# Kernel tuning notes

Hardware: AMD Instinct MI355X
Metric: run time of the kernel (lower is better)

Reference implementation:

```python
import jax, jax.numpy as jnp
import numpy as np

E, NH, NL, NP = 256, 8, 4, 4
D = E // NH
SPATIAL_SHAPES = np.array([[100, 134], [50, 67], [25, 34], [13, 17]], dtype=np.int64)
B = 2


def setup_inputs() -> dict:
    key = jax.random.key(0)
    ks = jax.random.split(key, 12)
    Lin = int((SPATIAL_SHAPES[:, 0] * SPATIAL_SHAPES[:, 1]).sum())
    Lq = Lin
    s = 0.02
    return {
        'query': jax.random.normal(ks[0], (Lq, B, E), jnp.float32),
        'value': jax.random.normal(ks[1], (Lin, B, E), jnp.float32),
        'reference_points': jax.random.uniform(ks[2], (B, Lq, NL, 2), jnp.float32),
        'spatial_shapes': SPATIAL_SHAPES,
        'W_value': jax.random.normal(ks[3], (E, E), jnp.float32) * s,
        'b_value': jnp.zeros((E,), jnp.float32),
        'W_offset': jax.random.normal(ks[4], (E, NH * NL * NP * 2), jnp.float32) * s,
        'b_offset': jax.random.normal(ks[5], (NH * NL * NP * 2,), jnp.float32) * 0.5,
        'W_attn': jax.random.normal(ks[6], (E, NH * NL * NP), jnp.float32) * s,
        'b_attn': jnp.zeros((NH * NL * NP,), jnp.float32),
        'W_out': jax.random.normal(ks[7], (E, E), jnp.float32) * s,
        'b_out': jnp.zeros((E,), jnp.float32),
    }


def _ms_deform_attn(value, spatial_shapes, sampling_locations, attention_weights):
    # value: (B, Lin, NH, D); sampling_locations: (B, Lq, NH, NL, NP, 2) in [0,1]
    # attention_weights: (B, Lq, NH, NL, NP)
    b, _, nh, d = value.shape
    lq = sampling_locations.shape[1]
    npnt = sampling_locations.shape[4]
    shapes = np.asarray(spatial_shapes)
    out = jnp.zeros((b, nh, lq, d), value.dtype)
    start = 0
    for l in range(shapes.shape[0]):
        H, W = int(shapes[l, 0]), int(shapes[l, 1])
        vl = value[:, start:start + H * W].transpose(0, 2, 1, 3)  # (B, NH, H*W, D)
        loc = sampling_locations[:, :, :, l].transpose(0, 2, 1, 3, 4)  # (B, NH, Lq, P, 2)
        # grid_sample align_corners=False convention (matches CUDA kernel)
        x = loc[..., 0] * W - 0.5
        y = loc[..., 1] * H - 0.5
        x0 = jnp.floor(x)
        y0 = jnp.floor(y)
        dx = x - x0
        dy = y - y0
        x0i = x0.astype(jnp.int32)
        y0i = y0.astype(jnp.int32)
        acc = jnp.zeros((b, nh, lq, npnt, d), value.dtype)
        corners = [
            (x0i, y0i, (1.0 - dx) * (1.0 - dy)),
            (x0i + 1, y0i, dx * (1.0 - dy)),
            (x0i, y0i + 1, (1.0 - dx) * dy),
            (x0i + 1, y0i + 1, dx * dy),
        ]
        for xi, yi, w in corners:
            valid = ((xi >= 0) & (xi < W) & (yi >= 0) & (yi < H)).astype(value.dtype)
            idx = jnp.clip(yi, 0, W - 1 if False else H - 1) * 0  # placeholder removed below
            idx = jnp.clip(yi, 0, H - 1) * W + jnp.clip(xi, 0, W - 1)  # (B, NH, Lq, P)
            g = jnp.take_along_axis(vl, idx.reshape(b, nh, -1)[..., None], axis=2)
            g = g.reshape(b, nh, lq, npnt, d)
            acc = acc + g * (w * valid)[..., None]
        awl = attention_weights[:, :, :, l].transpose(0, 2, 1, 3)  # (B, NH, Lq, P)
        out = out + jnp.einsum('bhqpd,bhqp->bhqd', acc, awl)
        start += H * W
    return out.transpose(0, 2, 1, 3).reshape(b, lq, nh * d)  # (B, Lq, E)


def reference(query, value, reference_points, spatial_shapes,
              W_value, b_value, W_offset, b_offset, W_attn, b_attn, W_out, b_out):
    q = query.transpose(1, 0, 2)   # (B, Lq, E)
    v = value.transpose(1, 0, 2)   # (B, Lin, E)
    b, lq, _ = q.shape
    lin = v.shape[1]
    v = (v @ W_value + b_value).reshape(b, lin, NH, D)
    offsets = (q @ W_offset + b_offset).reshape(b, lq, NH, NL, NP, 2)
    attn = (q @ W_attn + b_attn).reshape(b, lq, NH, NL, NP)
    attn = jax.nn.softmax(attn, axis=-1)  # softmax over points (as in source)
    shapes_f = jnp.asarray(np.asarray(spatial_shapes), jnp.float32)
    offset_normalizer = jnp.stack([shapes_f[:, 1], shapes_f[:, 0]], -1)  # (NL, 2) = (w, h)
    loc = reference_points[:, :, None, :, None, :] + offsets / offset_normalizer[None, None, None, :, None, :]
    out = _ms_deform_attn(v, spatial_shapes, loc, attn)  # (B, Lq, E)
    out = out @ W_out + b_out
    return out.transpose(1, 0, 2)  # (Lq, B, E)
```

## Files before the change

### kernel.cpp

```cpp
#include <hip/hip_runtime.h>
#include <math.h>

#define LQ    17821
#define MROWS 35642
#define KD    256

typedef __attribute__((ext_vector_type(8))) short bf16x8;
typedef __attribute__((ext_vector_type(4))) float f32x4;
typedef unsigned int u32;

__device__ __forceinline__ short f2bf(float f) {
  union { float f; unsigned u; } c; c.f = f;
  unsigned u = c.u;
  return (short)((u + 0x7fffu + ((u >> 16) & 1u)) >> 16);
}
__device__ __forceinline__ float bf2f(short s) {
  union { unsigned u; float f; } c;
  c.u = ((unsigned)(unsigned short)s) << 16;
  return c.f;
}

__device__ __forceinline__ void gld_lds16(const short* g, short* l) {
  __builtin_amdgcn_global_load_lds(
      (const __attribute__((address_space(1))) u32*)g,
      (__attribute__((address_space(3))) u32*)l, 16, 0, 0);
}

#define WAIT_VM4   { __builtin_amdgcn_s_waitcnt(0x0F74); asm volatile("" ::: "memory"); }
#define WAIT_VM0   { __builtin_amdgcn_s_waitcnt(0x0F70); asm volatile("" ::: "memory"); }
#define WAIT_LGKM0 { __builtin_amdgcn_s_waitcnt(0xC07F); asm volatile("" ::: "memory"); }
#define BARRIER    { asm volatile("" ::: "memory"); __builtin_amdgcn_s_barrier(); asm volatile("" ::: "memory"); }

__global__ __launch_bounds__(256) void prep(
    const float* __restrict__ query, const float* __restrict__ value,
    const float* __restrict__ Wv, const float* __restrict__ Woff,
    const float* __restrict__ Wat, const float* __restrict__ Wout,
    const float* __restrict__ boff, const float* __restrict__ bat,
    short* __restrict__ qb, short* __restrict__ vb,
    short* __restrict__ wT, float* __restrict__ fbias)
{
  const int y = blockIdx.y;
  if (y < 2) {
    const float* s = y ? value : query;
    short* d = y ? vb : qb;
    int i = (blockIdx.x * 256 + threadIdx.x) * 4;
    if (i < MROWS * KD) {
      float4 x = *(const float4*)(s + i);
      short4 o;
      o.x = f2bf(x.x); o.y = f2bf(x.y); o.z = f2bf(x.z); o.w = f2bf(x.w);
      *(short4*)(d + i) = o;
    }
    return;
  }
  int idx = blockIdx.x * 256 + threadIdx.x;
  if (idx < 229376) {
    const float* W; int base, N;
    if (idx < 65536)       { W = Wv;   base = 0;      N = 256; }
    else if (idx < 131072) { W = Woff; base = 65536;  N = 256; }
    else if (idx < 163840) { W = Wat;  base = 131072; N = 128; }
    else                   { W = Wout; base = 163840; N = 256; }
    int local = idx - base;
    int n = local >> 8, k = local & 255;
    wT[idx] = f2bf(W[k * N + n]);
  } else if (idx < 229376 + 384) {
    int j = idx - 229376;
    fbias[j] = (j < 256) ? boff[j] : bat[j - 256];
  }
}

template<bool O1BF>
__global__ __launch_bounds__(256) void gemm_pipe(
    const short* __restrict__ A0, const short* __restrict__ A1,
    const short* __restrict__ Bt0, const short* __restrict__ Bt1,
    const float* __restrict__ bias0, const float* __restrict__ bias1,
    short* __restrict__ out0, void* __restrict__ out1v,
    int N1, int gybase)
{
  __shared__ short As[2 * 128 * 32];
  __shared__ short Bs[2 * 128 * 32];

  const int tid = threadIdx.x;
  const int gy = blockIdx.y + gybase;
  const bool sel0 = gy < 2;
  const short* A = sel0 ? A0 : A1;
  const short* Bt = sel0 ? Bt0 : Bt1;
  const float* bias = sel0 ? bias0 : bias1;
  const int bn = (sel0 ? gy : gy - 2) * 128;
  const int bm = blockIdx.x * 128;

  const int wv = tid >> 6;
  const int lane = tid & 63;

  const int srow = lane >> 2;
  const int skel = (lane & 3) * 8;
  const int rA0 = min(bm + wv * 32 + srow, MROWS - 1);
  const int rA1 = min(bm + wv * 32 + 16 + srow, MROWS - 1);
  const short* gA0 = A + (size_t)rA0 * KD + skel;
  const short* gA1 = A + (size_t)rA1 * KD + skel;
  const short* gB0 = Bt + (size_t)(bn + wv * 32 + srow) * KD + skel;
  const short* gB1 = Bt + (size_t)(bn + wv * 32 + 16 + srow) * KD + skel;
  short* lA0 = &As[(wv * 32) * 32];
  short* lA1 = &As[(wv * 32 + 16) * 32];
  short* lB0 = &Bs[(wv * 32) * 32];
  short* lB1 = &Bs[(wv * 32 + 16) * 32];

#define ISSUE(t, buf)                          \
  {                                            \
    gld_lds16(gA0 + (t) * 32, lA0 + (buf) * 4096); \
    gld_lds16(gA1 + (t) * 32, lA1 + (buf) * 4096); \
    gld_lds16(gB0 + (t) * 32, lB0 + (buf) * 4096); \
    gld_lds16(gB1 + (t) * 32, lB1 + (buf) * 4096); \
  }

  const int wm = (wv & 1) * 64;
  const int wn = (wv >> 1) * 64;
  const int ln = lane & 15;
  const int lq = lane >> 4;

  f32x4 acc[4][4];
#pragma unroll
  for (int i = 0; i < 4; ++i)
#pragma unroll
    for (int j = 0; j < 4; ++j) acc[i][j] = (f32x4){0.f, 0.f, 0.f, 0.f};

  ISSUE(0, 0);
  ISSUE(1, 1);

#pragma unroll
  for (int t = 0; t < 8; ++t) {
    const int buf = t & 1;
    if (t < 7) { WAIT_VM4; } else { WAIT_VM0; }
    BARRIER;

    bf16x8 af[4], bfm[4];
#pragma unroll
    for (int i = 0; i < 4; ++i)
      af[i] = *(const bf16x8*)&As[buf * 4096 + (wm + i * 16 + ln) * 32 + lq * 8];
#pragma unroll
    for (int j = 0; j < 4; ++j)
      bfm[j] = *(const bf16x8*)&Bs[buf * 4096 + (wn + j * 16 + ln) * 32 + lq * 8];

    WAIT_LGKM0;
    BARRIER;
    if (t + 2 < 8) ISSUE(t + 2, buf);

#pragma unroll
    for (int i = 0; i < 4; ++i)
#pragma unroll
      for (int j = 0; j < 4; ++j)
        acc[i][j] = __builtin_amdgcn_mfma_f32_16x16x32_bf16(af[i], bfm[j], acc[i][j], 0, 0, 0);
  }
#undef ISSUE

  const int N = sel0 ? 256 : N1;
#pragma unroll
  for (int j = 0; j < 4; ++j) {
    const int col = bn + wn + j * 16 + ln;
    const float bb = bias[col];
#pragma unroll
    for (int i = 0; i < 4; ++i) {
      const int row0 = bm + wm + i * 16 + lq * 4;
#pragma unroll
      for (int r = 0; r < 4; ++r) {
        const int row = row0 + r;
        if (row < MROWS) {
          float v = acc[i][j][r] + bb;
          if (sel0)
            out0[(size_t)row * 256 + col] = f2bf(v);
          else if (O1BF)
            ((short*)out1v)[(size_t)row * N + col] = f2bf(v);
          else
            ((float*)out1v)[(size_t)row * N + col] = v;
        }
      }
    }
  }
}

__global__ __launch_bounds__(256) void msda_sample(
    const short* __restrict__ vproj, const short* __restrict__ oa,
    const float* __restrict__ refp, short* __restrict__ out)
{
  static constexpr int LVL_H[4] = {100, 50, 25, 13};
  static constexpr int LVL_W[4] = {134, 67, 34, 17};
  static constexpr int LVL_S[4] = {0, 13400, 16750, 17600};

  __shared__ uint4 s_pk[8 * 8 * 17];

  const int tid = threadIdx.x;
  const int m0 = blockIdx.x * 8;

#pragma unroll
  for (int it = 0; it < 4; ++it) {
    int w = tid + it * 256;
    int mr = w >> 7;
    int rest = w & 127;
    int h = rest >> 4;
    int lp = rest & 15;
    int l = lp >> 2;
    int p = lp & 3;
    int m = m0 + mr;
    if (m < MROWS) {
      int b = m & 1, q = m >> 1;
      const int Hl = LVL_H[l], Wl = LVL_W[l], Sl = LVL_S[l];
      const float fW = (float)Wl, fH = (float)Hl;

      short4 a4 = *(const short4*)(oa + (size_t)m * 384 + 256 + h * 16 + l * 4);
      float a0 = bf2f(a4.x), a1 = bf2f(a4.y), a2 = bf2f(a4.z), a3 = bf2f(a4.w);
      float mx = fmaxf(fmaxf(a0, a1), fmaxf(a2, a3));
      a0 = __expf(a0 - mx); a1 = __expf(a1 - mx);
      a2 = __expf(a2 - mx); a3 = __expf(a3 - mx);
      float sel = (p == 0) ? a0 : (p == 1) ? a1 : (p == 2) ? a2 : a3;
      float aw = sel / (a0 + a1 + a2 + a3);

      const short* oPtr = oa + (size_t)m * 384 + h * 32 + l * 8 + p * 2;
      float ox = bf2f(oPtr[0]), oy = bf2f(oPtr[1]);
      const float* rPtr = refp + ((size_t)b * LQ + q) * 8 + l * 2;
      float rx = rPtr[0], ry = rPtr[1];

      float x = (rx + ox / fW) * fW - 0.5f;
      float y = (ry + oy / fH) * fH - 0.5f;
      float x0f = floorf(x), y0f = floorf(y);
      float dx = x - x0f, dy = y - y0f;
      int x0 = (int)x0f, y0 = (int)y0f;
      int x1 = x0 + 1, y1 = y0 + 1;

      float w00 = (1.f - dx) * (1.f - dy) * aw;
      float w10 = dx * (1.f - dy) * aw;
      float w01 = (1.f - dx) * dy * aw;
      float w11 = dx * dy * aw;

      bool vx0 = (x0 >= 0) & (x0 < Wl);
      bool vx1 = (x1 >= 0) & (x1 < Wl);
      bool vy0 = (y0 >= 0) & (y0 < Hl);
      bool vy1 = (y1 >= 0) & (y1 < Hl);
      int cx0 = min(max(x0, 0), Wl - 1);
      int cx1 = min(max(x1, 0), Wl - 1);
      int cy0 = min(max(y0, 0), Hl - 1);
      int cy1 = min(max(y1, 0), Hl - 1);

      int r0 = Sl + cy0 * Wl;
      int r1 = Sl + cy1 * Wl;

      float f00 = (vy0 & vx0) ? w00 : 0.f;
      float f10 = (vy0 & vx1) ? w10 : 0.f;
      float f01 = (vy1 & vx0) ? w01 : 0.f;
      float f11 = (vy1 & vx1) ? w11 : 0.f;
      u32 pk0 = (u32)((r0 + cx0) * 2 + b) |
                ((u32)__builtin_bit_cast(unsigned short, (_Float16)f00) << 16);
      u32 pk1 = (u32)((r0 + cx1) * 2 + b) |
                ((u32)__builtin_bit_cast(unsigned short, (_Float16)f10) << 16);
      u32 pk2 = (u32)((r1 + cx0) * 2 + b) |
                ((u32)__builtin_bit_cast(unsigned short, (_Float16)f01) << 16);
      u32 pk3 = (u32)((r1 + cx1) * 2 + b) |
                ((u32)__builtin_bit_cast(unsigned short, (_Float16)f11) << 16);
      int e = (mr * 8 + h) * 17 + lp;
      s_pk[e] = make_uint4(pk0, pk1, pk2, pk3);
    }
  }
  __syncthreads();

  const int mr = tid >> 5;
  const int t = tid & 31;
  const int h = t >> 2;
  const int dq = t & 3;
  const int m = m0 + mr;
  if (m >= MROWS) return;

  const int laneOff = h * 32 + dq * 8;
  const int ebase = (mr * 8 + h) * 17;
  const short* vp = vproj + laneOff;

  float acc[8];
#pragma unroll
  for (int e = 0; e < 8; ++e) acc[e] = 0.f;

#pragma unroll 4
  for (int lp = 0; lp < 16; ++lp) {
    uint4 pk = s_pk[ebase + lp];
    bf16x8 u00 = *(const bf16x8*)(vp + ((int)(pk.x & 0xFFFFu) << 8));
    bf16x8 u10 = *(const bf16x8*)(vp + ((int)(pk.y & 0xFFFFu) << 8));
    bf16x8 u01 = *(const bf16x8*)(vp + ((int)(pk.z & 0xFFFFu) << 8));
    bf16x8 u11 = *(const bf16x8*)(vp + ((int)(pk.w & 0xFFFFu) << 8));
    float w0 = (float)__builtin_bit_cast(_Float16, (unsigned short)(pk.x >> 16));
    float w1 = (float)__builtin_bit_cast(_Float16, (unsigned short)(pk.y >> 16));
    float w2 = (float)__builtin_bit_cast(_Float16, (unsigned short)(pk.z >> 16));
    float w3 = (float)__builtin_bit_cast(_Float16, (unsigned short)(pk.w >> 16));
#pragma unroll
    for (int e = 0; e < 8; ++e) {
      acc[e] = fmaf(w0, bf2f(u00[e]), acc[e]);
      acc[e] = fmaf(w1, bf2f(u10[e]), acc[e]);
      acc[e] = fmaf(w2, bf2f(u01[e]), acc[e]);
      acc[e] = fmaf(w3, bf2f(u11[e]), acc[e]);
    }
  }

  bf16x8 o;
#pragma unroll
  for (int e = 0; e < 8; ++e) o[e] = f2bf(acc[e]);
  *(bf16x8*)(out + (size_t)m * 256 + laneOff) = o;
}

extern "C" void kernel_launch(void* const* d_in, const int* in_sizes, int n_in,
                              void* d_out, int out_size, void* d_ws, size_t ws_size,
                              hipStream_t stream)
{
  const float* query = (const float*)d_in[0];
  const float* value = (const float*)d_in[1];
  const float* refp  = (const float*)d_in[2];
  const float* Wv   = (const float*)d_in[4];
  const float* bv   = (const float*)d_in[5];
  const float* Woff = (const float*)d_in[6];
  const float* boff = (const float*)d_in[7];
  const float* Wat  = (const float*)d_in[8];
  const float* bat  = (const float*)d_in[9];
  const float* Wout = (const float*)d_in[10];
  const float* bout = (const float*)d_in[11];
  float* out = (float*)d_out;

  const size_t NELT = (size_t)MROWS * 256;
  short* wT    = (short*)d_ws;
  float* fbias = (float*)(wT + 229376);
  short* qb    = (short*)(fbias + 384);
  short* vb    = qb + NELT;
  short* vproj = vb + NELT;
  short* oa    = vproj + NELT;
  short* accb  = vb;

  dim3 blk(256, 1, 1);
  int gm = (MROWS + 127) / 128;

  prep<<<dim3(8911, 3), blk, 0, stream>>>(
      query, value, Wv, Woff, Wat, Wout, boff, bat, qb, vb, wT, fbias);

  gemm_pipe<true><<<dim3(gm, 5), blk, 0, stream>>>(
      vb, qb, wT, wT + 65536, bv, fbias, vproj, oa, 384, 0);

  msda_sample<<<dim3((MROWS + 7) / 8), blk, 0, stream>>>(vproj, oa, refp, accb);

  gemm_pipe<false><<<dim3(gm, 2), blk, 0, stream>>>(
      accb, accb, wT + 163840, wT + 163840, bout, bout, nullptr, out, 256, 2);
}
```

Baseline: 282.8 us.

## Fuse fp32-to-bf16 conversion of query/value into the input GEMM loads

Result: no change. 280.3 us (-0.9%).

```diff
diff --git a/kernel.cpp b/kernel.cpp
--- a/kernel.cpp
+++ b/kernel.cpp
@@ -26,32 +26,18 @@
       (__attribute__((address_space(3))) u32*)l, 16, 0, 0);
 }
 
+#define WAIT_VM6   { __builtin_amdgcn_s_waitcnt(0x0F76); asm volatile("" ::: "memory"); }
 #define WAIT_VM4   { __builtin_amdgcn_s_waitcnt(0x0F74); asm volatile("" ::: "memory"); }
 #define WAIT_VM0   { __builtin_amdgcn_s_waitcnt(0x0F70); asm volatile("" ::: "memory"); }
 #define WAIT_LGKM0 { __builtin_amdgcn_s_waitcnt(0xC07F); asm volatile("" ::: "memory"); }
 #define BARRIER    { asm volatile("" ::: "memory"); __builtin_amdgcn_s_barrier(); asm volatile("" ::: "memory"); }
 
-__global__ __launch_bounds__(256) void prep(
-    const float* __restrict__ query, const float* __restrict__ value,
+__global__ __launch_bounds__(256) void prep_w(
     const float* __restrict__ Wv, const float* __restrict__ Woff,
     const float* __restrict__ Wat, const float* __restrict__ Wout,
     const float* __restrict__ boff, const float* __restrict__ bat,
-    short* __restrict__ qb, short* __restrict__ vb,
     short* __restrict__ wT, float* __restrict__ fbias)
 {
-  const int y = blockIdx.y;
-  if (y < 2) {
-    const float* s = y ? value : query;
-    short* d = y ? vb : qb;
-    int i = (blockIdx.x * 256 + threadIdx.x) * 4;
-    if (i < MROWS * KD) {
-      float4 x = *(const float4*)(s + i);
-      short4 o;
-      o.x = f2bf(x.x); o.y = f2bf(x.y); o.z = f2bf(x.z); o.w = f2bf(x.w);
-      *(short4*)(d + i) = o;
-    }
-    return;
-  }
   int idx = blockIdx.x * 256 + threadIdx.x;
   if (idx < 229376) {
     const float* W; int base, N;
@@ -68,9 +54,9 @@
   }
 }
 
-template<bool O1BF>
+template<bool O1BF, bool AFP32>
 __global__ __launch_bounds__(256) void gemm_pipe(
-    const short* __restrict__ A0, const short* __restrict__ A1,
+    const void* __restrict__ A0v, const void* __restrict__ A1v,
     const short* __restrict__ Bt0, const short* __restrict__ Bt1,
     const float* __restrict__ bias0, const float* __restrict__ bias1,
     short* __restrict__ out0, void* __restrict__ out1v,
@@ -82,7 +68,6 @@
   const int tid = threadIdx.x;
   const int gy = blockIdx.y + gybase;
   const bool sel0 = gy < 2;
-  const short* A = sel0 ? A0 : A1;
   const short* Bt = sel0 ? Bt0 : Bt1;
   const float* bias = sel0 ? bias0 : bias1;
   const int bn = (sel0 ? gy : gy - 2) * 128;
@@ -95,21 +80,59 @@
   const int skel = (lane & 3) * 8;
   const int rA0 = min(bm + wv * 32 + srow, MROWS - 1);
   const int rA1 = min(bm + wv * 32 + 16 + srow, MROWS - 1);
-  const short* gA0 = A + (size_t)rA0 * KD + skel;
-  const short* gA1 = A + (size_t)rA1 * KD + skel;
+
   const short* gB0 = Bt + (size_t)(bn + wv * 32 + srow) * KD + skel;
   const short* gB1 = Bt + (size_t)(bn + wv * 32 + 16 + srow) * KD + skel;
+  short* lB0 = &Bs[(wv * 32) * 32];
+  short* lB1 = &Bs[(wv * 32 + 16) * 32];
+
+  const short* gA0 = nullptr; const short* gA1 = nullptr;
   short* lA0 = &As[(wv * 32) * 32];
   short* lA1 = &As[(wv * 32 + 16) * 32];
-  short* lB0 = &Bs[(wv * 32) * 32];
-  short* lB1 = &Bs[(wv * 32 + 16) * 32];
-
-#define ISSUE(t, buf)                          \
-  {                                            \
-    gld_lds16(gA0 + (t) * 32, lA0 + (buf) * 4096); \
-    gld_lds16(gA1 + (t) * 32, lA1 + (buf) * 4096); \
-    gld_lds16(gB0 + (t) * 32, lB0 + (buf) * 4096); \
-    gld_lds16(gB1 + (t) * 32, lB1 + (buf) * 4096); \
+  const float* gAf0 = nullptr; const float* gAf1 = nullptr;
+  short* wA0 = &As[(wv * 32 + srow) * 32 + skel];
+  short* wA1 = &As[(wv * 32 + 16 + srow) * 32 + skel];
+
+  if constexpr (AFP32) {
+    const float* A = sel0 ? (const float*)A0v : (const float*)A1v;
+    gAf0 = A + (size_t)rA0 * KD + skel;
+    gAf1 = A + (size_t)rA1 * KD + skel;
+  } else {
+    const short* A = sel0 ? (const short*)A0v : (const short*)A1v;
+    gA0 = A + (size_t)rA0 * KD + skel;
+    gA1 = A + (size_t)rA1 * KD + skel;
+  }
+
+#define BISSUE(t, buf)                               \
+  {                                                  \
+    gld_lds16(gB0 + (t) * 32, lB0 + (buf) * 4096);   \
+    gld_lds16(gB1 + (t) * 32, lB1 + (buf) * 4096);   \
+  }
+#define AISSUE_BF(t, buf)                            \
+  {                                                  \
+    gld_lds16(gA0 + (t) * 32, lA0 + (buf) * 4096);   \
+    gld_lds16(gA1 + (t) * 32, lA1 + (buf) * 4096);   \
+  }
+#define ALOAD(s, t)                                  \
+  {                                                  \
+    ar[s][0] = *(const float4*)(gAf0 + (t) * 32);    \
+    ar[s][1] = *(const float4*)(gAf0 + (t) * 32 + 4);\
+    ar[s][2] = *(const float4*)(gAf1 + (t) * 32);    \
+    ar[s][3] = *(const float4*)(gAf1 + (t) * 32 + 4);\
+  }
+#define AWRITE(s, buf)                                                        \
+  {                                                                           \
+    bf16x8 w0, w1;                                                            \
+    w0[0]=f2bf(ar[s][0].x); w0[1]=f2bf(ar[s][0].y);                           \
+    w0[2]=f2bf(ar[s][0].z); w0[3]=f2bf(ar[s][0].w);                           \
+    w0[4]=f2bf(ar[s][1].x); w0[5]=f2bf(ar[s][1].y);                           \
+    w0[6]=f2bf(ar[s][1].z); w0[7]=f2bf(ar[s][1].w);                           \
+    w1[0]=f2bf(ar[s][2].x); w1[1]=f2bf(ar[s][2].y);                           \
+    w1[2]=f2bf(ar[s][2].z); w1[3]=f2bf(ar[s][2].w);                           \
+    w1[4]=f2bf(ar[s][3].x); w1[5]=f2bf(ar[s][3].y);                           \
+    w1[6]=f2bf(ar[s][3].z); w1[7]=f2bf(ar[s][3].w);                           \
+    *(bf16x8*)(wA0 + (buf) * 4096) = w0;                                      \
+    *(bf16x8*)(wA1 + (buf) * 4096) = w1;                                      \
   }
 
   const int wm = (wv & 1) * 64;
@@ -123,14 +146,28 @@
 #pragma unroll
     for (int j = 0; j < 4; ++j) acc[i][j] = (f32x4){0.f, 0.f, 0.f, 0.f};
 
-  ISSUE(0, 0);
-  ISSUE(1, 1);
+  float4 ar[2][4];
+
+  if constexpr (AFP32) {
+    ALOAD(0, 0); BISSUE(0, 0);
+    ALOAD(1, 1); BISSUE(1, 1);
+    AWRITE(0, 0);
+  } else {
+    AISSUE_BF(0, 0); BISSUE(0, 0);
+    AISSUE_BF(1, 1); BISSUE(1, 1);
+  }
 
 #pragma unroll
   for (int t = 0; t < 8; ++t) {
     const int buf = t & 1;
-    if (t < 7) { WAIT_VM4; } else { WAIT_VM0; }
-    BARRIER;
+    if constexpr (AFP32) {
+      if (t < 7) { WAIT_VM6; } else { WAIT_VM0; }
+      WAIT_LGKM0;
+      BARRIER;
+    } else {
+      if (t < 7) { WAIT_VM4; } else { WAIT_VM0; }
+      BARRIER;
+    }
 
     bf16x8 af[4], bfm[4];
 #pragma unroll
@@ -142,15 +179,25 @@
 
     WAIT_LGKM0;
     BARRIER;
-    if (t + 2 < 8) ISSUE(t + 2, buf);
+    if (t + 2 < 8) {
+      if constexpr (AFP32) { ALOAD((t & 1), t + 2); BISSUE(t + 2, buf); }
+      else                 { AISSUE_BF(t + 2, buf); BISSUE(t + 2, buf); }
+    }
 
 #pragma unroll
     for (int i = 0; i < 4; ++i)
 #pragma unroll
       for (int j = 0; j < 4; ++j)
         acc[i][j] = __builtin_amdgcn_mfma_f32_16x16x32_bf16(af[i], bfm[j], acc[i][j], 0, 0, 0);
-  }
-#undef ISSUE
+
+    if constexpr (AFP32) {
+      if (t < 7) AWRITE(((t + 1) & 1), (buf ^ 1));
+    }
+  }
+#undef BISSUE
+#undef AISSUE_BF
+#undef ALOAD
+#undef AWRITE
 
   const int N = sel0 ? 256 : N1;
 #pragma unroll
@@ -330,14 +377,13 @@
   dim3 blk(256, 1, 1);
   int gm = (MROWS + 127) / 128;
 
-  prep<<<dim3(8911, 3), blk, 0, stream>>>(
-      query, value, Wv, Woff, Wat, Wout, boff, bat, qb, vb, wT, fbias);
-
-  gemm_pipe<true><<<dim3(gm, 5), blk, 0, stream>>>(
-      vb, qb, wT, wT + 65536, bv, fbias, vproj, oa, 384, 0);
+  prep_w<<<dim3(898), blk, 0, stream>>>(Wv, Woff, Wat, Wout, boff, bat, wT, fbias);
+
+  gemm_pipe<true, true><<<dim3(gm, 5), blk, 0, stream>>>(
+      value, query, wT, wT + 65536, bv, fbias, vproj, oa, 384, 0);
 
   msda_sample<<<dim3((MROWS + 7) / 8), blk, 0, stream>>>(vproj, oa, refp, accb);
 
-  gemm_pipe<false><<<dim3(gm, 2), blk, 0, stream>>>(
+  gemm_pipe<false, false><<<dim3(gm, 2), blk, 0, stream>>>(
       accb, accb, wT + 163840, wT + 163840, bout, bout, nullptr, out, 256, 2);
 }
```

## Double GEMM K-tile to 64 with XOR-swizzled LDS layout

Applied to the files above, without the earlier changes.

After: 292.2 us. 3.3% more time.

```diff
diff --git a/kernel.cpp b/kernel.cpp
--- a/kernel.cpp
+++ b/kernel.cpp
@@ -26,7 +26,7 @@
       (__attribute__((address_space(3))) u32*)l, 16, 0, 0);
 }
 
-#define WAIT_VM4   { __builtin_amdgcn_s_waitcnt(0x0F74); asm volatile("" ::: "memory"); }
+#define WAIT_VM8   { __builtin_amdgcn_s_waitcnt(0x0F78); asm volatile("" ::: "memory"); }
 #define WAIT_VM0   { __builtin_amdgcn_s_waitcnt(0x0F70); asm volatile("" ::: "memory"); }
 #define WAIT_LGKM0 { __builtin_amdgcn_s_waitcnt(0xC07F); asm volatile("" ::: "memory"); }
 #define BARRIER    { asm volatile("" ::: "memory"); __builtin_amdgcn_s_barrier(); asm volatile("" ::: "memory"); }
@@ -76,8 +76,8 @@
     short* __restrict__ out0, void* __restrict__ out1v,
     int N1, int gybase)
 {
-  __shared__ short As[2 * 128 * 32];
-  __shared__ short Bs[2 * 128 * 32];
+  __shared__ short As[2 * 128 * 64];
+  __shared__ short Bs[2 * 128 * 64];
 
   const int tid = threadIdx.x;
   const int gy = blockIdx.y + gybase;
@@ -91,31 +91,55 @@
   const int wv = tid >> 6;
   const int lane = tid & 63;
 
-  const int srow = lane >> 2;
-  const int skel = (lane & 3) * 8;
-  const int rA0 = min(bm + wv * 32 + srow, MROWS - 1);
-  const int rA1 = min(bm + wv * 32 + 16 + srow, MROWS - 1);
-  const short* gA0 = A + (size_t)rA0 * KD + skel;
-  const short* gA1 = A + (size_t)rA1 * KD + skel;
-  const short* gB0 = Bt + (size_t)(bn + wv * 32 + srow) * KD + skel;
-  const short* gB1 = Bt + (size_t)(bn + wv * 32 + 16 + srow) * KD + skel;
-  short* lA0 = &As[(wv * 32) * 32];
-  short* lA1 = &As[(wv * 32 + 16) * 32];
-  short* lB0 = &Bs[(wv * 32) * 32];
-  short* lB1 = &Bs[(wv * 32 + 16) * 32];
-
-#define ISSUE(t, buf)                          \
-  {                                            \
-    gld_lds16(gA0 + (t) * 32, lA0 + (buf) * 4096); \
-    gld_lds16(gA1 + (t) * 32, lA1 + (buf) * 4096); \
-    gld_lds16(gB0 + (t) * 32, lB0 + (buf) * 4096); \
-    gld_lds16(gB1 + (t) * 32, lB1 + (buf) * 4096); \
-  }
+  const int srow = lane >> 3;
+  const int slot = lane & 7;
+  const int kel_sw = ((slot ^ srow) << 3);
+
+  const short* gA[4]; const short* gB[4];
+  short* lA[4]; short* lB[4];
+#pragma unroll
+  for (int g = 0; g < 4; ++g) {
+    int rA = min(bm + wv * 32 + g * 8 + srow, MROWS - 1);
+    gA[g] = A + (size_t)rA * KD + kel_sw;
+    gB[g] = Bt + (size_t)(bn + wv * 32 + g * 8 + srow) * KD + kel_sw;
+    lA[g] = &As[(wv * 32 + g * 8) * 64];
+    lB[g] = &Bs[(wv * 32 + g * 8) * 64];
+  }
+
+#define ISSUE(t, buf)                                    \
+  { gld_lds16(gA[0] + (t) * 64, lA[0] + (buf) * 8192);   \
+    gld_lds16(gA[1] + (t) * 64, lA[1] + (buf) * 8192);   \
+    gld_lds16(gA[2] + (t) * 64, lA[2] + (buf) * 8192);   \
+    gld_lds16(gA[3] + (t) * 64, lA[3] + (buf) * 8192);   \
+    gld_lds16(gB[0] + (t) * 64, lB[0] + (buf) * 8192);   \
+    gld_lds16(gB[1] + (t) * 64, lB[1] + (buf) * 8192);   \
+    gld_lds16(gB[2] + (t) * 64, lB[2] + (buf) * 8192);   \
+    gld_lds16(gB[3] + (t) * 64, lB[3] + (buf) * 8192); }
 
   const int wm = (wv & 1) * 64;
   const int wn = (wv >> 1) * 64;
   const int ln = lane & 15;
   const int lq = lane >> 4;
+  const int rsw = ln & 7;
+
+#define KSTEP(ks)                                                             \
+  {                                                                           \
+    bf16x8 af[4], bfm[4];                                                     \
+    _Pragma("unroll")                                                         \
+    for (int i = 0; i < 4; ++i)                                               \
+      af[i] = *(const bf16x8*)&As[buf * 8192 + (wm + i * 16 + ln) * 64 +      \
+                                  ((((ks) * 4 + lq) ^ rsw) * 8)];             \
+    _Pragma("unroll")                                                         \
+    for (int j = 0; j < 4; ++j)                                               \
+      bfm[j] = *(const bf16x8*)&Bs[buf * 8192 + (wn + j * 16 + ln) * 64 +     \
+                                   ((((ks) * 4 + lq) ^ rsw) * 8)];            \
+    _Pragma("unroll")                                                         \
+    for (int i = 0; i < 4; ++i)                                               \
+      _Pragma("unroll")                                                       \
+      for (int j = 0; j < 4; ++j)                                             \
+        acc[i][j] = __builtin_amdgcn_mfma_f32_16x16x32_bf16(                  \
+            af[i], bfm[j], acc[i][j], 0, 0, 0);                               \
+  }
 
   f32x4 acc[4][4];
 #pragma unroll
@@ -127,30 +151,20 @@
   ISSUE(1, 1);
 
 #pragma unroll
-  for (int t = 0; t < 8; ++t) {
+  for (int t = 0; t < 4; ++t) {
     const int buf = t & 1;
-    if (t < 7) { WAIT_VM4; } else { WAIT_VM0; }
+    if (t < 3) { WAIT_VM8; } else { WAIT_VM0; }
     BARRIER;
 
-    bf16x8 af[4], bfm[4];
-#pragma unroll
-    for (int i = 0; i < 4; ++i)
-      af[i] = *(const bf16x8*)&As[buf * 4096 + (wm + i * 16 + ln) * 32 + lq * 8];
-#pragma unroll
-    for (int j = 0; j < 4; ++j)
-      bfm[j] = *(const bf16x8*)&Bs[buf * 4096 + (wn + j * 16 + ln) * 32 + lq * 8];
+    KSTEP(0);
+    KSTEP(1);
 
     WAIT_LGKM0;
     BARRIER;
-    if (t + 2 < 8) ISSUE(t + 2, buf);
-
-#pragma unroll
-    for (int i = 0; i < 4; ++i)
-#pragma unroll
-      for (int j = 0; j < 4; ++j)
-        acc[i][j] = __builtin_amdgcn_mfma_f32_16x16x32_bf16(af[i], bfm[j], acc[i][j], 0, 0, 0);
+    if (t + 2 < 4) ISSUE(t + 2, buf);
   }
 #undef ISSUE
+#undef KSTEP
 
   const int N = sel0 ? 256 : N1;
 #pragma unroll
```

## Fuse fp32-to-bf16 input conversion into projection GEMM with resident A tile

Applied to the files above, without the earlier changes.

Measured after the change: 290.8 us. 2.8% more time.

```diff
diff --git a/kernel.cpp b/kernel.cpp
--- a/kernel.cpp
+++ b/kernel.cpp
@@ -27,31 +27,17 @@
 }
 
 #define WAIT_VM4   { __builtin_amdgcn_s_waitcnt(0x0F74); asm volatile("" ::: "memory"); }
+#define WAIT_VM2   { __builtin_amdgcn_s_waitcnt(0x0F72); asm volatile("" ::: "memory"); }
 #define WAIT_VM0   { __builtin_amdgcn_s_waitcnt(0x0F70); asm volatile("" ::: "memory"); }
 #define WAIT_LGKM0 { __builtin_amdgcn_s_waitcnt(0xC07F); asm volatile("" ::: "memory"); }
 #define BARRIER    { asm volatile("" ::: "memory"); __builtin_amdgcn_s_barrier(); asm volatile("" ::: "memory"); }
 
-__global__ __launch_bounds__(256) void prep(
-    const float* __restrict__ query, const float* __restrict__ value,
+__global__ __launch_bounds__(256) void prep_w(
     const float* __restrict__ Wv, const float* __restrict__ Woff,
     const float* __restrict__ Wat, const float* __restrict__ Wout,
     const float* __restrict__ boff, const float* __restrict__ bat,
-    short* __restrict__ qb, short* __restrict__ vb,
     short* __restrict__ wT, float* __restrict__ fbias)
 {
-  const int y = blockIdx.y;
-  if (y < 2) {
-    const float* s = y ? value : query;
-    short* d = y ? vb : qb;
-    int i = (blockIdx.x * 256 + threadIdx.x) * 4;
-    if (i < MROWS * KD) {
-      float4 x = *(const float4*)(s + i);
-      short4 o;
-      o.x = f2bf(x.x); o.y = f2bf(x.y); o.z = f2bf(x.z); o.w = f2bf(x.w);
-      *(short4*)(d + i) = o;
-    }
-    return;
-  }
   int idx = blockIdx.x * 256 + threadIdx.x;
   if (idx < 229376) {
     const float* W; int base, N;
@@ -66,6 +52,120 @@
     int j = idx - 229376;
     fbias[j] = (j < 256) ? boff[j] : bat[j - 256];
   }
+}
+
+__global__ __launch_bounds__(256) void gemm_fused_in(
+    const float* __restrict__ value, const float* __restrict__ query,
+    const short* __restrict__ wT, const float* __restrict__ bv,
+    const float* __restrict__ fbias,
+    short* __restrict__ vproj, short* __restrict__ oa)
+{
+  __shared__ short As[128 * 256];
+  __shared__ short Bs[2 * 128 * 32];
+
+  const int tid = threadIdx.x;
+  const int s1 = blockIdx.y;
+  const float* Af = s1 ? query : value;
+  const short* Bt = s1 ? (wT + 65536) : wT;
+  const float* bias = s1 ? fbias : bv;
+  const int NB = s1 ? 3 : 2;
+  const int NW = s1 ? 384 : 256;
+  short* outp = s1 ? oa : vproj;
+  const int bm = blockIdx.x * 128;
+
+#pragma unroll 4
+  for (int k = 0; k < 16; ++k) {
+    int c = tid + k * 256;
+    int row = c >> 5, s = c & 31;
+    int gr = min(bm + row, MROWS - 1);
+    const float* src = Af + (size_t)gr * KD + s * 8;
+    float4 x0 = *(const float4*)src;
+    float4 x1 = *(const float4*)(src + 4);
+    bf16x8 w;
+    w[0] = f2bf(x0.x); w[1] = f2bf(x0.y); w[2] = f2bf(x0.z); w[3] = f2bf(x0.w);
+    w[4] = f2bf(x1.x); w[5] = f2bf(x1.y); w[6] = f2bf(x1.z); w[7] = f2bf(x1.w);
+    int ps = (s & 16) | ((s ^ row) & 15);
+    *(bf16x8*)&As[row * 256 + ps * 8] = w;
+  }
+  __syncthreads();
+
+  const int wv = tid >> 6;
+  const int lane = tid & 63;
+  const int srow = lane >> 2;
+  const int skel = (lane & 3) * 8;
+  short* lB0 = &Bs[(wv * 32) * 32];
+  short* lB1 = &Bs[(wv * 32 + 16) * 32];
+
+  const int wm = (wv & 1) * 64;
+  const int wn = (wv >> 1) * 64;
+  const int ln = lane & 15;
+  const int lq = lane >> 4;
+
+#define ISSUEB(t, buf)                              \
+  {                                                 \
+    gld_lds16(gB0 + (t) * 32, lB0 + (buf) * 4096);  \
+    gld_lds16(gB1 + (t) * 32, lB1 + (buf) * 4096);  \
+  }
+
+  for (int bnI = 0; bnI < NB; ++bnI) {
+    const int bn = bnI * 128;
+    const short* gB0 = Bt + (size_t)(bn + wv * 32 + srow) * KD + skel;
+    const short* gB1 = gB0 + (size_t)16 * KD;
+
+    f32x4 acc[4][4];
+#pragma unroll
+    for (int i = 0; i < 4; ++i)
+#pragma unroll
+      for (int j = 0; j < 4; ++j) acc[i][j] = (f32x4){0.f, 0.f, 0.f, 0.f};
+
+    ISSUEB(0, 0);
+    ISSUEB(1, 1);
+
+#pragma unroll
+    for (int t = 0; t < 8; ++t) {
+      const int buf = t & 1;
+      if (t < 7) { WAIT_VM2; } else { WAIT_VM0; }
+      BARRIER;
+
+      bf16x8 af[4], bfm[4];
+#pragma unroll
+      for (int i = 0; i < 4; ++i) {
+        const int L = t * 4 + lq;
+        const int ps = (L & 16) | ((L ^ ln) & 15);
+        af[i] = *(const bf16x8*)&As[(wm + i * 16 + ln) * 256 + ps * 8];
+      }
+#pragma unroll
+      for (int j = 0; j < 4; ++j)
+        bfm[j] = *(const bf16x8*)&Bs[buf * 4096 + (wn + j * 16 + ln) * 32 + lq * 8];
+
+      WAIT_LGKM0;
+      BARRIER;
+      if (t + 2 < 8) ISSUEB(t + 2, buf);
+
+#pragma unroll
+      for (int i = 0; i < 4; ++i)
+#pragma unroll
+        for (int j = 0; j < 4; ++j)
+          acc[i][j] = __builtin_amdgcn_mfma_f32_16x16x32_bf16(af[i], bfm[j], acc[i][j], 0, 0, 0);
+    }
+
+#pragma unroll
+    for (int j = 0; j < 4; ++j) {
+      const int col = bn + wn + j * 16 + ln;
+      const float bb = bias[col];
+#pragma unroll
+      for (int i = 0; i < 4; ++i) {
+        const int row0 = bm + wm + i * 16 + lq * 4;
+#pragma unroll
+        for (int r = 0; r < 4; ++r) {
+          const int row = row0 + r;
+          if (row < MROWS)
+            outp[(size_t)row * NW + col] = f2bf(acc[i][j][r] + bb);
+        }
+      }
+    }
+  }
+#undef ISSUEB
 }
 
 template<bool O1BF>
@@ -321,20 +421,17 @@
   const size_t NELT = (size_t)MROWS * 256;
   short* wT    = (short*)d_ws;
   float* fbias = (float*)(wT + 229376);
-  short* qb    = (short*)(fbias + 384);
-  short* vb    = qb + NELT;
-  short* vproj = vb + NELT;
+  short* vproj = (short*)(fbias + 384);
   short* oa    = vproj + NELT;
-  short* accb  = vb;
+  short* accb  = oa + (size_t)MROWS * 384;
 
   dim3 blk(256, 1, 1);
   int gm = (MROWS + 127) / 128;
 
-  prep<<<dim3(8911, 3), blk, 0, stream>>>(
-      query, value, Wv, Woff, Wat, Wout, boff, bat, qb, vb, wT, fbias);
-
-  gemm_pipe<true><<<dim3(gm, 5), blk, 0, stream>>>(
-      vb, qb, wT, wT + 65536, bv, fbias, vproj, oa, 384, 0);
+  prep_w<<<dim3(898), blk, 0, stream>>>(Wv, Woff, Wat, Wout, boff, bat, wT, fbias);
+
+  gemm_fused_in<<<dim3(gm, 2), blk, 0, stream>>>(
+      value, query, wT, bv, fbias, vproj, oa);
 
   msda_sample<<<dim3((MROWS + 7) / 8), blk, 0, stream>>>(vproj, oa, refp, accb);
 
```
